# Performance work log

Measured on AMD Instinct MI355X. Metric: run time of the kernel, lower is better.

The kernel has to match this reference:

```python
import jax, jax.numpy as jnp
import numpy as np

N_HEADS, D_MODEL, D_HEAD, N_CTX = 16, 2048, 128, 2048
BATCH, SEQ = 2, 2048
ATTN_SCALE = float(np.sqrt(D_HEAD))
IGNORE = -100000.0


def setup_inputs() -> dict:
    key = jax.random.key(0)
    ks = jax.random.split(key, 6)
    init = 0.02
    return {
        "residual": jax.random.normal(ks[0], (BATCH, SEQ, D_MODEL), dtype=jnp.float32),
        "x": jax.random.normal(ks[1], (BATCH, SEQ, D_MODEL), dtype=jnp.float32),
        "W_Q": jax.random.normal(ks[2], (N_HEADS, D_MODEL, D_HEAD), dtype=jnp.float32) * init,
        "W_K": jax.random.normal(ks[3], (N_HEADS, D_MODEL, D_HEAD), dtype=jnp.float32) * init,
        "W_V": jax.random.normal(ks[4], (N_HEADS, D_MODEL, D_HEAD), dtype=jnp.float32) * init,
        "W_O": jax.random.normal(ks[5], (N_HEADS, D_HEAD, D_MODEL), dtype=jnp.float32) * init,
        "b_Q": jnp.zeros((N_HEADS, D_HEAD), dtype=jnp.float32),
        "b_K": jnp.zeros((N_HEADS, D_HEAD), dtype=jnp.float32),
        "b_V": jnp.zeros((N_HEADS, D_HEAD), dtype=jnp.float32),
        "b_O": jnp.zeros((D_MODEL,), dtype=jnp.float32),
    }


def reference(residual, x, W_Q, W_K, W_V, W_O, b_Q, b_K, b_V, b_O):
    # use_split_qkv_input=False: QKV all read from residual
    q = jnp.einsum('bpm,hmd->bphd', residual, W_Q) + b_Q  # [b, pos, h, d_head]
    k = jnp.einsum('bpm,hmd->bphd', residual, W_K) + b_K
    v = jnp.einsum('bpm,hmd->bphd', residual, W_V) + b_V
    attn_scores = jnp.einsum('bqhd,bkhd->bhqk', q, k) / ATTN_SCALE  # [b, h, q, k]
    key_len = attn_scores.shape[-1]
    mask = jnp.tril(jnp.ones((key_len, key_len), dtype=bool))  # causal mask [q, k]
    attn_scores = jnp.where(mask, attn_scores, IGNORE)
    pattern = jax.nn.softmax(attn_scores, axis=-1)
    z = jnp.einsum('bkhd,bhqk->bqhd', v, pattern)
    out = jnp.einsum('bphd,hdm->bpm', z, W_O) + b_O
    return (residual, out)
```

## Files before the change

kernel.cpp:

```cpp
#include <hip/hip_runtime.h>
#include <hip/hip_bf16.h>

typedef __attribute__((ext_vector_type(8))) short bf16x8;
typedef __attribute__((ext_vector_type(4))) float f32x4;

#define N_HEADS 16
#define D_MODEL 2048
#define D_HEAD  128
#define SEQ     2048
#define BATCH   2
#define HD      (N_HEADS * D_HEAD)
#define QSCALE  0.08838834764831845f

__device__ inline __hip_bfloat16 to_bf16(float v) { return __float2bfloat16(v); }
__device__ inline __hip_bfloat16 to_bf16(__hip_bfloat16 v) { return v; }

typedef __attribute__((address_space(3))) unsigned lds_u32_t;
typedef __attribute__((address_space(1))) unsigned glb_u32_t;
__device__ inline void async16(void* l, const void* g) {
    __builtin_amdgcn_global_load_lds((const glb_u32_t*)g, (lds_u32_t*)l, 16, 0, 0);
}

__global__ __launch_bounds__(256) void cvt_dual(
    const float4* __restrict__ in, float4* __restrict__ o32,
    __hip_bfloat16* __restrict__ obf, long n4)
{
    for (long i = (long)blockIdx.x * blockDim.x + threadIdx.x; i < n4;
         i += (long)gridDim.x * blockDim.x) {
        float4 v = in[i];
        o32[i] = v;
        union { __hip_bfloat16 b[4]; uint2 u; } p;
        p.b[0] = __float2bfloat16(v.x);
        p.b[1] = __float2bfloat16(v.y);
        p.b[2] = __float2bfloat16(v.z);
        p.b[3] = __float2bfloat16(v.w);
        *(uint2*)(obf + 4 * i) = p.u;
    }
}

template <typename Tin>
__global__ __launch_bounds__(256) void transpose_to_bf16(
    const Tin* __restrict__ in, __hip_bfloat16* __restrict__ out,
    int R, int C, long in_rs, long in_bs, long out_bs)
{
    __shared__ Tin tile[64][65];
    const Tin* src = in + (long)blockIdx.z * in_bs;
    __hip_bfloat16* dst = out + (long)blockIdx.z * out_bs;
    const int c0 = blockIdx.x * 64, r0 = blockIdx.y * 64;
    const int t = threadIdx.x;
    const int tr = t >> 4;
    const int tc = (t & 15) * 4;
#pragma unroll
    for (int i = 0; i < 4; i++) {
        int r = tr + i * 16;
#pragma unroll
        for (int j = 0; j < 4; j++)
            tile[r][tc + j] = src[(long)(r0 + r) * in_rs + c0 + tc + j];
    }
    __syncthreads();
#pragma unroll
    for (int i = 0; i < 4; i++) {
        int c = tr + i * 16;
#pragma unroll
        for (int j = 0; j < 4; j++)
            dst[(long)(c0 + c) * R + r0 + tc + j] = to_bf16(tile[tc + j][c]);
    }
}

__device__ inline void store_out(__hip_bfloat16* p, float v) { *p = __float2bfloat16(v); }
__device__ inline void store_out(float* p, float v) { *p = v; }

template <typename OutT>
__global__ __launch_bounds__(256) void gemm_qkv(
    const __hip_bfloat16* __restrict__ A,
    const __hip_bfloat16* __restrict__ WTbase,
    const float* __restrict__ bQ, const float* bK, const float* bV,
    OutT* __restrict__ Cbase,
    int M, int N, int K, long wstride, long cstride, float scale0)
{
    __shared__ __align__(16) __hip_bfloat16 As[128 * 32];
    __shared__ __align__(16) __hip_bfloat16 Bs[128 * 32];
    const int z = blockIdx.z;
    const __hip_bfloat16* Bt = WTbase + (long)z * wstride;
    const float* bias = (z == 0) ? bQ : ((z == 1) ? bK : bV);
    OutT* C = Cbase + (long)z * cstride;
    const float outscale = (z == 0) ? scale0 : 1.0f;

    const int tid = threadIdx.x;
    const int lane = tid & 63, wave = tid >> 6;
    const int l15 = lane & 15, quad = lane >> 4;
    const int wr = wave >> 1, wc = wave & 1;
    const int m0 = blockIdx.y * 128, n0 = blockIdx.x * 128;

    const short* Ap = (const short*)A;
    const short* Bp = (const short*)Bt;

    f32x4 acc[4][4] = {};

    for (int k0 = 0; k0 < K; k0 += 32) {
        __syncthreads();
#pragma unroll
        for (int i = 0; i < 2; i++) {
            int e = i * 256 + tid;
            int row = e >> 2, ch = e & 3;
            async16((char*)As + (i * 256 + wave * 64) * 16,
                    Ap + (long)(m0 + row) * K + k0 + ch * 8);
            async16((char*)Bs + (i * 256 + wave * 64) * 16,
                    Bp + (long)(n0 + row) * K + k0 + ch * 8);
        }
        __syncthreads();

        bf16x8 af[4], bfr[4];
#pragma unroll
        for (int t = 0; t < 4; t++) {
            af[t]  = *(const bf16x8*)((const short*)As + (wr * 64 + t * 16 + l15) * 32 + quad * 8);
            bfr[t] = *(const bf16x8*)((const short*)Bs + (wc * 64 + t * 16 + l15) * 32 + quad * 8);
        }
#pragma unroll
        for (int i = 0; i < 4; i++)
#pragma unroll
            for (int j = 0; j < 4; j++)
                acc[i][j] = __builtin_amdgcn_mfma_f32_16x16x32_bf16(af[i], bfr[j], acc[i][j], 0, 0, 0);
    }

    const int mw = m0 + wr * 64, nw = n0 + wc * 64;
#pragma unroll
    for (int i = 0; i < 4; i++) {
#pragma unroll
        for (int j = 0; j < 4; j++) {
            int n = nw + j * 16 + l15;
            float bv = bias[n];
#pragma unroll
            for (int r = 0; r < 4; r++) {
                int m = mw + i * 16 + quad * 4 + r;
                store_out(&C[(long)m * N + n], (acc[i][j][r] + bv) * outscale);
            }
        }
    }
}

template <typename OutT>
__global__ __launch_bounds__(256, 2) void gemm128(
    const __hip_bfloat16* __restrict__ A,
    const __hip_bfloat16* __restrict__ WTbase,
    const float* __restrict__ bQ, const float* bK, const float* bV,
    OutT* __restrict__ Cbase,
    int N, int K, long wstride, long cstride, float scale0,
    int nx, int ny)
{
    __shared__ __align__(16) short lds[2][2][128 * 64];

    const int tid = threadIdx.x;
    const int lane = tid & 63;
    const int wave = tid >> 6;
    const int l15 = lane & 15, quad = lane >> 4, l7 = lane & 7;
    const int wm = wave >> 1, wn = wave & 1;

    const int nwg = gridDim.x;
    const int orig = blockIdx.x;
    const int wg = (orig & 7) * (nwg >> 3) + (orig >> 3);
    const int nxy = nx * ny;
    const int z = wg / nxy;
    const int rem = wg - z * nxy;
    const int by = rem / nx;
    const int bx = rem - by * nx;
    const int m0 = by * 128, n0 = bx * 128;

    const short* Ap = (const short*)A;
    const short* Bp = (const short*)WTbase + (long)z * wstride;

    const int rsub = lane >> 3;
    const int c0 = (lane & 7) ^ rsub;

    auto stage = [&](int bf, int reg, const short* gbase, int kt) {
        char* base = (char*)&lds[bf][reg][0];
        const short* g = gbase + (long)kt * 64;
#pragma unroll
        for (int s = 0; s < 4; s++) {
            int row = (s * 4 + wave) * 8 + rsub;
            async16(base + (s * 4 + wave) * 1024, g + (long)row * K + c0 * 8);
        }
    };

    const short* Agbl = Ap + (long)m0 * K;
    const short* Bgbl = Bp + (long)n0 * K;

    const int NT = K >> 6;

    stage(0, 0, Agbl, 0); stage(0, 1, Bgbl, 0);
    stage(1, 0, Agbl, 1);
    asm volatile("s_waitcnt vmcnt(4)" ::: "memory");
    __builtin_amdgcn_s_barrier();

    f32x4 acc[4][4] = {};
    const int ar0 = wm * 64;
    const int br0 = wn * 64;

#pragma unroll 2
    for (int u = 0; u < NT; ++u) {
        asm volatile("" ::: "memory");
        const int bf = u & 1, bo = bf ^ 1;
        const short* la = &lds[bf][0][0];
        const short* lb = &lds[bf][1][0];

        bf16x8 a[4][2], b0[2][2], b1[2][2];

#pragma unroll
        for (int fm = 0; fm < 4; fm++)
#pragma unroll
            for (int kk = 0; kk < 2; kk++)
                a[fm][kk] = *(const bf16x8*)(la + (ar0 + fm * 16 + l15) * 64
                                             + (((kk * 4 + quad) ^ l7) * 8));
#pragma unroll
        for (int fn = 0; fn < 2; fn++)
#pragma unroll
            for (int kk = 0; kk < 2; kk++)
                b0[fn][kk] = *(const bf16x8*)(lb + (br0 + fn * 16 + l15) * 64
                                              + (((kk * 4 + quad) ^ l7) * 8));
        if (u + 1 < NT) stage(bo, 1, Bgbl, u + 1);
        __builtin_amdgcn_s_barrier();
        asm volatile("s_waitcnt lgkmcnt(0)" ::: "memory");
        __builtin_amdgcn_sched_barrier(0);
        __builtin_amdgcn_s_setprio(1);
#pragma unroll
        for (int fm = 0; fm < 4; fm++)
#pragma unroll
            for (int fn = 0; fn < 2; fn++)
#pragma unroll
                for (int kk = 0; kk < 2; kk++)
                    acc[fm][fn] = __builtin_amdgcn_mfma_f32_16x16x32_bf16(
                        a[fm][kk], b0[fn][kk], acc[fm][fn], 0, 0, 0);
        __builtin_amdgcn_s_setprio(0);
        __builtin_amdgcn_s_barrier();

#pragma unroll
        for (int fn = 0; fn < 2; fn++)
#pragma unroll
            for (int kk = 0; kk < 2; kk++)
                b1[fn][kk] = *(const bf16x8*)(lb + (br0 + 32 + fn * 16 + l15) * 64
                                              + (((kk * 4 + quad) ^ l7) * 8));
        if (u + 2 < NT) stage(bf, 0, Agbl, u + 2);
        __builtin_amdgcn_s_barrier();
        asm volatile("s_waitcnt lgkmcnt(0)" ::: "memory");
        __builtin_amdgcn_sched_barrier(0);
        __builtin_amdgcn_s_setprio(1);
#pragma unroll
        for (int fm = 0; fm < 4; fm++)
#pragma unroll
            for (int fn = 0; fn < 2; fn++)
#pragma unroll
                for (int kk = 0; kk < 2; kk++)
                    acc[fm][2 + fn] = __builtin_amdgcn_mfma_f32_16x16x32_bf16(
                        a[fm][kk], b1[fn][kk], acc[fm][2 + fn], 0, 0, 0);
        __builtin_amdgcn_s_setprio(0);
        if (u + 2 < NT) {
            asm volatile("s_waitcnt vmcnt(4)" ::: "memory");
        } else if (u + 1 < NT) {
            asm volatile("s_waitcnt vmcnt(0)" ::: "memory");
        }
        __builtin_amdgcn_s_barrier();
    }

    const float* bias = (z == 0) ? bQ : ((z == 1) ? bK : bV);
    OutT* C = Cbase + (long)z * cstride;
    const float outscale = (z == 0) ? scale0 : 1.0f;
#pragma unroll
    for (int mi = 0; mi < 4; mi++) {
#pragma unroll
        for (int nj = 0; nj < 4; nj++) {
            const int n = n0 + wn * 64 + nj * 16 + l15;
            const float bv = bias[n];
#pragma unroll
            for (int r = 0; r < 4; r++) {
                const int m = m0 + wm * 64 + mi * 16 + quad * 4 + r;
                store_out(&C[(long)m * N + n], (acc[mi][nj][r] + bv) * outscale);
            }
        }
    }
}

__global__ __launch_bounds__(256) void attn_fused(
    const __hip_bfloat16* Q,
    const __hip_bfloat16* __restrict__ Kin,
    const __hip_bfloat16* __restrict__ Vt,
    __hip_bfloat16* Z)
{
    __shared__ __align__(16) __hip_bfloat16 Ks[64 * 128];
    __shared__ __align__(16) __hip_bfloat16 Vs[128 * 64];
    __shared__ __align__(16) __hip_bfloat16 pbuf[4][32 * 72];

    const int tid = threadIdx.x;
    const int lane = tid & 63, wave = tid >> 6;
    const int l15 = lane & 15, quad = lane >> 4;

    const int g0id = blockIdx.x;
    const int qt = (g0id < 256) ? (15 - (g0id & 15)) : (g0id & 15);
    const int hb = ((g0id >> 4) & 15) + ((g0id >> 8) << 4);
    const int b = hb >> 4, h = hb & 15;

    const short* Qp = (const short*)Q;
    const short* Kp = (const short*)Kin;
    const short* Vp = (const short*)Vt;

    bf16x8 aq[2][4];
#pragma unroll
    for (int g = 0; g < 2; g++)
#pragma unroll
        for (int ks = 0; ks < 4; ks++)
            aq[g][ks] = *(const bf16x8*)(Qp + (long)(b * SEQ + qt * 128 + g * 64 + wave * 16 + l15) * HD
                                         + h * D_HEAD + ks * 32 + quad * 8);

    f32x4 o[2][8] = {};
    float lsum[2][4] = {};

    const short* pw = (const short*)pbuf[wave];

    const int ktiles = 2 * qt + 2;
    for (int kt = 0; kt < ktiles; kt++) {
        const int kb = kt * 64;
        __syncthreads();
#pragma unroll
        for (int i = 0; i < 4; i++) {
            int e = i * 256 + tid;
            int row = e >> 4, cc = (e & 15) ^ (row & 7);
            async16((char*)Ks + (size_t)e * 16,
                    Kp + (long)(b * SEQ + kb + row) * HD + h * D_HEAD + cc * 8);
        }
#pragma unroll
        for (int i = 0; i < 4; i++) {
            int e = i * 256 + tid;
            int row = e >> 3, cc = (e & 7) ^ (row & 7);
            async16((char*)Vs + (size_t)e * 16,
                    Vp + ((long)(b * N_HEADS + h) * D_HEAD + row) * SEQ + kb + cc * 8);
        }
        __syncthreads();

        f32x4 s[2][4] = {};
#pragma unroll
        for (int nt = 0; nt < 4; nt++)
#pragma unroll
            for (int ks = 0; ks < 4; ks++) {
                bf16x8 bk = *(const bf16x8*)((const short*)Ks + (nt * 16 + l15) * 128
                                             + (((ks * 4 + quad) ^ (l15 & 7)) * 8));
                s[0][nt] = __builtin_amdgcn_mfma_f32_16x16x32_bf16(aq[0][ks], bk, s[0][nt], 0, 0, 0);
                s[1][nt] = __builtin_amdgcn_mfma_f32_16x16x32_bf16(aq[1][ks], bk, s[1][nt], 0, 0, 0);
            }

#pragma unroll
        for (int g = 0; g < 2; g++) {
            if (kt >= 2 * qt + g) {
                bool full = kt > 2 * qt + g;
#pragma unroll
                for (int nt = 0; nt < 4; nt++)
#pragma unroll
                    for (int r = 0; r < 4; r++) {
                        int qq = wave * 16 + quad * 4 + r;
                        int kk = nt * 16 + l15;
                        if (full || kk > qq) s[g][nt][r] = -100000.0f;
                    }
            }
        }

#pragma unroll
        for (int g = 0; g < 2; g++) {
#pragma unroll
            for (int nt = 0; nt < 4; nt++)
#pragma unroll
                for (int r = 0; r < 4; r++) {
                    float p = __expf(s[g][nt][r]);
                    s[g][nt][r] = p;
                    lsum[g][r] += p;
                    pbuf[wave][(g * 16 + quad * 4 + r) * 72 + nt * 16 + l15] = __float2bfloat16(p);
                }
        }

#pragma unroll
        for (int ks2 = 0; ks2 < 2; ks2++) {
            bf16x8 ap0 = *(const bf16x8*)(pw + (0  + l15) * 72 + ks2 * 32 + quad * 8);
            bf16x8 ap1 = *(const bf16x8*)(pw + (16 + l15) * 72 + ks2 * 32 + quad * 8);
#pragma unroll
            for (int tj = 0; tj < 8; tj++) {
                bf16x8 bv = *(const bf16x8*)((const short*)Vs + (tj * 16 + l15) * 64
                                             + (((ks2 * 4 + quad) ^ (l15 & 7)) * 8));
                o[0][tj] = __builtin_amdgcn_mfma_f32_16x16x32_bf16(ap0, bv, o[0][tj], 0, 0, 0);
                o[1][tj] = __builtin_amdgcn_mfma_f32_16x16x32_bf16(ap1, bv, o[1][tj], 0, 0, 0);
            }
        }
    }

#pragma unroll
    for (int g = 0; g < 2; g++) {
        float inv[4];
#pragma unroll
        for (int r = 0; r < 4; r++) {
            float v = lsum[g][r];
#pragma unroll
            for (int ofs = 1; ofs < 16; ofs <<= 1)
                v += __shfl_xor(v, ofs, 64);
            inv[r] = 1.0f / v;
        }
#pragma unroll
        for (int tj = 0; tj < 8; tj++)
#pragma unroll
            for (int r = 0; r < 4; r++) {
                long q = b * SEQ + qt * 128 + g * 64 + wave * 16 + quad * 4 + r;
                Z[q * HD + h * D_HEAD + tj * 16 + l15] = __float2bfloat16(o[g][tj][r] * inv[r]);
            }
    }
}

extern "C" void kernel_launch(void* const* d_in, const int* in_sizes, int n_in,
                              void* d_out, int out_size, void* d_ws, size_t ws_size,
                              hipStream_t stream)
{
    const float* residual = (const float*)d_in[0];
    const float* W_Q = (const float*)d_in[2];
    const float* W_K = (const float*)d_in[3];
    const float* W_V = (const float*)d_in[4];
    const float* W_O = (const float*)d_in[5];
    const float* b_Q = (const float*)d_in[6];
    const float* b_K = (const float*)d_in[7];
    const float* b_V = (const float*)d_in[8];
    const float* b_O = (const float*)d_in[9];
    float* out = (float*)d_out;

    const long TOK = (long)BATCH * SEQ;
    const long TD = TOK * D_MODEL;
    const long WSZ = (long)D_MODEL * D_MODEL;
    char* ws = (char*)d_ws;
    __hip_bfloat16* Qb = (__hip_bfloat16*)(ws);
    __hip_bfloat16* Kb = (__hip_bfloat16*)(ws + TD * 2);
    __hip_bfloat16* Vb = (__hip_bfloat16*)(ws + TD * 4);
    __hip_bfloat16* Rb = (__hip_bfloat16*)(ws + TD * 6);
    __hip_bfloat16* Vt = Rb;
    __hip_bfloat16* WT = (__hip_bfloat16*)(ws + TD * 8);
    __hip_bfloat16* Zb = Qb;

    const size_t NEED_BIG = (size_t)TD * 8 + (size_t)WSZ * 2 * 3;
    const bool big = ws_size >= NEED_BIG;

    dim3 tB(256);

    cvt_dual<<<2048, tB, 0, stream>>>((const float4*)residual, (float4*)out, Rb, TD / 4);

    dim3 gridWqkv(D_HEAD / 64, D_MODEL / 64, N_HEADS);
    const float* Wqkv[3] = {W_Q, W_K, W_V};
    const float* bqkv[3] = {b_Q, b_K, b_V};

    if (big) {
        for (int z = 0; z < 3; z++)
            transpose_to_bf16<float><<<gridWqkv, tB, 0, stream>>>(
                Wqkv[z], WT + (long)z * WSZ, D_MODEL, D_HEAD,
                D_HEAD, (long)D_MODEL * D_HEAD, (long)D_HEAD * D_MODEL);
        gemm128<__hip_bfloat16><<<dim3(1536), dim3(256), 0, stream>>>(
            Rb, WT, b_Q, b_K, b_V, Qb, D_MODEL, D_MODEL,
            WSZ, TD, QSCALE, D_MODEL / 128, (int)(TOK / 128));
    } else {
        dim3 gridG(D_MODEL / 128, (int)(TOK / 128), 1);
        for (int z = 0; z < 3; z++) {
            transpose_to_bf16<float><<<gridWqkv, tB, 0, stream>>>(
                Wqkv[z], WT, D_MODEL, D_HEAD,
                D_HEAD, (long)D_MODEL * D_HEAD, (long)D_HEAD * D_MODEL);
            gemm_qkv<__hip_bfloat16><<<gridG, tB, 0, stream>>>(
                Rb, WT, bqkv[z], bqkv[z], bqkv[z], Qb + (long)z * TD,
                (int)TOK, D_MODEL, D_MODEL, 0, 0, z == 0 ? QSCALE : 1.0f);
        }
    }

    dim3 gridVt(D_HEAD / 64, SEQ / 64, N_HEADS);
    for (int b = 0; b < BATCH; b++) {
        transpose_to_bf16<__hip_bfloat16><<<gridVt, tB, 0, stream>>>(
            Vb + (long)b * SEQ * D_MODEL, Vt + (long)b * N_HEADS * D_HEAD * SEQ,
            SEQ, D_HEAD, (long)D_MODEL, (long)D_HEAD, (long)D_HEAD * SEQ);
    }

    attn_fused<<<dim3(512), dim3(256), 0, stream>>>(Qb, Kb, Vt, Zb);

    dim3 gridWo(D_MODEL / 64, D_MODEL / 64, 1);
    transpose_to_bf16<float><<<gridWo, tB, 0, stream>>>(
        W_O, WT, D_MODEL, D_MODEL, (long)D_MODEL, 0, 0);
    if (big) {
        gemm128<float><<<dim3(512), dim3(256), 0, stream>>>(
            Zb, WT, b_O, b_O, b_O, out + TD, D_MODEL, D_MODEL,
            0, 0, 1.0f, D_MODEL / 128, (int)(TOK / 128));
    } else {
        dim3 gridO(D_MODEL / 128, (int)(TOK / 128), 1);
        gemm_qkv<float><<<gridO, tB, 0, stream>>>(
            Zb, WT, b_O, b_O, b_O, out + TD, (int)TOK, D_MODEL, D_MODEL, 0, 0, 1.0f);
    }
}
```

Baseline: 430.6 us.

## Split attention block across eight waves, one 16-row query slice each

The attention kernel now launches 512 threads per block, and each of the eight waves owns a single 16-row query group instead of two groups per wave across four waves. This halves per-wave register state (Q fragments, O accumulators, row sums), which should allow higher occupancy. It also lets the first-half waves skip the final fully masked key tile instead of computing it and overwriting it with the mask value. The trade-off is that each K/V tile loaded to LDS is reused by fewer MFMAs per wave, and the block-wide barriers now synchronize more waves, some of which sit idle on the last tile.

```diff
diff --git a/kernel.cpp b/kernel.cpp
--- a/kernel.cpp
+++ b/kernel.cpp
@@ -279,7 +279,7 @@
     }
 }
 
-__global__ __launch_bounds__(256) void attn_fused(
+__global__ __launch_bounds__(512, 4) void attn_fused(
     const __hip_bfloat16* Q,
     const __hip_bfloat16* __restrict__ Kin,
     const __hip_bfloat16* __restrict__ Vt,
@@ -287,11 +287,13 @@
 {
     __shared__ __align__(16) __hip_bfloat16 Ks[64 * 128];
     __shared__ __align__(16) __hip_bfloat16 Vs[128 * 64];
-    __shared__ __align__(16) __hip_bfloat16 pbuf[4][32 * 72];
+    __shared__ __align__(16) __hip_bfloat16 pbuf[8][16 * 80];
 
     const int tid = threadIdx.x;
     const int lane = tid & 63, wave = tid >> 6;
     const int l15 = lane & 15, quad = lane >> 4;
+    const int wh = wave >> 2;
+    const int rr4 = (wave & 3) * 16 + quad * 4;
 
     const int g0id = blockIdx.x;
     const int qt = (g0id < 256) ? (15 - (g0id & 15)) : (g0id & 15);
@@ -302,16 +304,14 @@
     const short* Kp = (const short*)Kin;
     const short* Vp = (const short*)Vt;
 
-    bf16x8 aq[2][4];
-#pragma unroll
-    for (int g = 0; g < 2; g++)
-#pragma unroll
-        for (int ks = 0; ks < 4; ks++)
-            aq[g][ks] = *(const bf16x8*)(Qp + (long)(b * SEQ + qt * 128 + g * 64 + wave * 16 + l15) * HD
-                                         + h * D_HEAD + ks * 32 + quad * 8);
-
-    f32x4 o[2][8] = {};
-    float lsum[2][4] = {};
+    bf16x8 aq[4];
+#pragma unroll
+    for (int ks = 0; ks < 4; ks++)
+        aq[ks] = *(const bf16x8*)(Qp + (long)(b * SEQ + qt * 128 + wave * 16 + l15) * HD
+                                  + h * D_HEAD + ks * 32 + quad * 8);
+
+    f32x4 o[8] = {};
+    float lsum[4] = {};
 
     const short* pw = (const short*)pbuf[wave];
 
@@ -320,93 +320,80 @@
         const int kb = kt * 64;
         __syncthreads();
 #pragma unroll
-        for (int i = 0; i < 4; i++) {
-            int e = i * 256 + tid;
+        for (int i = 0; i < 2; i++) {
+            int e = i * 512 + tid;
             int row = e >> 4, cc = (e & 15) ^ (row & 7);
             async16((char*)Ks + (size_t)e * 16,
                     Kp + (long)(b * SEQ + kb + row) * HD + h * D_HEAD + cc * 8);
         }
 #pragma unroll
-        for (int i = 0; i < 4; i++) {
-            int e = i * 256 + tid;
+        for (int i = 0; i < 2; i++) {
+            int e = i * 512 + tid;
             int row = e >> 3, cc = (e & 7) ^ (row & 7);
             async16((char*)Vs + (size_t)e * 16,
                     Vp + ((long)(b * N_HEADS + h) * D_HEAD + row) * SEQ + kb + cc * 8);
         }
         __syncthreads();
 
-        f32x4 s[2][4] = {};
-#pragma unroll
-        for (int nt = 0; nt < 4; nt++)
-#pragma unroll
-            for (int ks = 0; ks < 4; ks++) {
-                bf16x8 bk = *(const bf16x8*)((const short*)Ks + (nt * 16 + l15) * 128
-                                             + (((ks * 4 + quad) ^ (l15 & 7)) * 8));
-                s[0][nt] = __builtin_amdgcn_mfma_f32_16x16x32_bf16(aq[0][ks], bk, s[0][nt], 0, 0, 0);
-                s[1][nt] = __builtin_amdgcn_mfma_f32_16x16x32_bf16(aq[1][ks], bk, s[1][nt], 0, 0, 0);
-            }
-
-#pragma unroll
-        for (int g = 0; g < 2; g++) {
-            if (kt >= 2 * qt + g) {
-                bool full = kt > 2 * qt + g;
+        if (kt <= 2 * qt + wh) {
+            f32x4 s[4] = {};
+#pragma unroll
+            for (int nt = 0; nt < 4; nt++)
+#pragma unroll
+                for (int ks = 0; ks < 4; ks++) {
+                    bf16x8 bk = *(const bf16x8*)((const short*)Ks + (nt * 16 + l15) * 128
+                                                 + (((ks * 4 + quad) ^ (l15 & 7)) * 8));
+                    s[nt] = __builtin_amdgcn_mfma_f32_16x16x32_bf16(aq[ks], bk, s[nt], 0, 0, 0);
+                }
+
+            if (kt == 2 * qt + wh) {
 #pragma unroll
                 for (int nt = 0; nt < 4; nt++)
 #pragma unroll
                     for (int r = 0; r < 4; r++) {
-                        int qq = wave * 16 + quad * 4 + r;
                         int kk = nt * 16 + l15;
-                        if (full || kk > qq) s[g][nt][r] = -100000.0f;
+                        if (kk > rr4 + r) s[nt][r] = -100000.0f;
                     }
             }
-        }
-
-#pragma unroll
-        for (int g = 0; g < 2; g++) {
+
 #pragma unroll
             for (int nt = 0; nt < 4; nt++)
 #pragma unroll
                 for (int r = 0; r < 4; r++) {
-                    float p = __expf(s[g][nt][r]);
-                    s[g][nt][r] = p;
-                    lsum[g][r] += p;
-                    pbuf[wave][(g * 16 + quad * 4 + r) * 72 + nt * 16 + l15] = __float2bfloat16(p);
+                    float p = __expf(s[nt][r]);
+                    lsum[r] += p;
+                    pbuf[wave][(quad * 4 + r) * 80 + nt * 16 + l15] = __float2bfloat16(p);
                 }
-        }
-
-#pragma unroll
-        for (int ks2 = 0; ks2 < 2; ks2++) {
-            bf16x8 ap0 = *(const bf16x8*)(pw + (0  + l15) * 72 + ks2 * 32 + quad * 8);
-            bf16x8 ap1 = *(const bf16x8*)(pw + (16 + l15) * 72 + ks2 * 32 + quad * 8);
-#pragma unroll
-            for (int tj = 0; tj < 8; tj++) {
-                bf16x8 bv = *(const bf16x8*)((const short*)Vs + (tj * 16 + l15) * 64
-                                             + (((ks2 * 4 + quad) ^ (l15 & 7)) * 8));
-                o[0][tj] = __builtin_amdgcn_mfma_f32_16x16x32_bf16(ap0, bv, o[0][tj], 0, 0, 0);
-                o[1][tj] = __builtin_amdgcn_mfma_f32_16x16x32_bf16(ap1, bv, o[1][tj], 0, 0, 0);
+
+#pragma unroll
+            for (int ks2 = 0; ks2 < 2; ks2++) {
+                bf16x8 ap = *(const bf16x8*)(pw + l15 * 80 + ks2 * 32 + quad * 8);
+#pragma unroll
+                for (int tj = 0; tj < 8; tj++) {
+                    bf16x8 bv = *(const bf16x8*)((const short*)Vs + (tj * 16 + l15) * 64
+                                                 + (((ks2 * 4 + quad) ^ (l15 & 7)) * 8));
+                    o[tj] = __builtin_amdgcn_mfma_f32_16x16x32_bf16(ap, bv, o[tj], 0, 0, 0);
+                }
             }
         }
     }
 
-#pragma unroll
-    for (int g = 0; g < 2; g++) {
-        float inv[4];
+    float inv[4];
+#pragma unroll
+    for (int r = 0; r < 4; r++) {
+        float v = lsum[r];
+#pragma unroll
+        for (int ofs = 1; ofs < 16; ofs <<= 1)
+            v += __shfl_xor(v, ofs, 64);
+        inv[r] = 1.0f / v;
+    }
+#pragma unroll
+    for (int tj = 0; tj < 8; tj++)
 #pragma unroll
         for (int r = 0; r < 4; r++) {
-            float v = lsum[g][r];
-#pragma unroll
-            for (int ofs = 1; ofs < 16; ofs <<= 1)
-                v += __shfl_xor(v, ofs, 64);
-            inv[r] = 1.0f / v;
-        }
-#pragma unroll
-        for (int tj = 0; tj < 8; tj++)
-#pragma unroll
-            for (int r = 0; r < 4; r++) {
-                long q = b * SEQ + qt * 128 + g * 64 + wave * 16 + quad * 4 + r;
-                Z[q * HD + h * D_HEAD + tj * 16 + l15] = __float2bfloat16(o[g][tj][r] * inv[r]);
-            }
-    }
+            long q = b * SEQ + qt * 128 + wave * 16 + quad * 4 + r;
+            Z[q * HD + h * D_HEAD + tj * 16 + l15] = __float2bfloat16(o[tj][r] * inv[r]);
+        }
 }
 
 extern "C" void kernel_launch(void* const* d_in, const int* in_sizes, int n_in,
@@ -474,7 +461,7 @@
             SEQ, D_HEAD, (long)D_MODEL, (long)D_HEAD, (long)D_HEAD * SEQ);
     }
 
-    attn_fused<<<dim3(512), dim3(256), 0, stream>>>(Qb, Kb, Vt, Zb);
+    attn_fused<<<dim3(512), dim3(512), 0, stream>>>(Qb, Kb, Vt, Zb);
 
     dim3 gridWo(D_MODEL / 64, D_MODEL / 64, 1);
     transpose_to_bf16<float><<<gridWo, tB, 0, stream>>>(
```

Result: faster. 398.2 us (-7.5%).
